# Kernel optimization log

Measured on AMD Instinct MI355X. Metric: run time of the kernel, lower is better.

## Reference

```python
import jax, jax.numpy as jnp
import numpy as np

B, T, D, H = 4, 1024, 1024, 16
DH = D // H
NEG_BIG = jnp.float32(-2.0**32 + 1)


def layer_norm(x, scale, bias, eps=1e-5):
    mean = jnp.mean(x, axis=-1, keepdims=True)
    var = jnp.mean(jnp.square(x - mean), axis=-1, keepdims=True)
    return (x - mean) * jax.lax.rsqrt(var + eps) * scale + bias


def setup_inputs() -> dict:
    key = jax.random.key(0)
    ks = jax.random.split(key, 10)
    s = 0.02
    x = jax.random.normal(ks[0], (B, T, D), jnp.float32)
    mask = jax.random.randint(ks[1], (B, T), 0, 2).astype(jnp.float32)
    return {
        "x": x,
        "mask": mask,
        "wq": jax.random.normal(ks[2], (D, D), jnp.float32) * s,
        "wk": jax.random.normal(ks[3], (D, D), jnp.float32) * s,
        "wv": jax.random.normal(ks[4], (D, D), jnp.float32) * s,
        "w1": jax.random.normal(ks[5], (D, D), jnp.float32) * s,
        "b1": jnp.zeros((D,), jnp.float32),
        "w2": jax.random.normal(ks[6], (D, D), jnp.float32) * s,
        "b2": jnp.zeros((D,), jnp.float32),
        "ln1_s": jnp.ones((D,), jnp.float32),
        "ln1_b": jnp.zeros((D,), jnp.float32),
        "ln2_s": jnp.ones((D,), jnp.float32),
        "ln2_b": jnp.zeros((D,), jnp.float32),
        "ln3_s": jnp.ones((D,), jnp.float32),
        "ln3_b": jnp.zeros((D,), jnp.float32),
    }


def _mask_enc(x, mask, wq, wk, wv, w1, b1, w2, b2,
              ln1_s, ln1_b, ln2_s, ln2_b, ln3_s, ln3_b):
    b, t, d = x.shape
    # --- multi-head attention (hand-rolled, matches torch split/cat trick) ---
    Q = (x @ wq).reshape(b, t, H, DH).transpose(0, 2, 1, 3)  # [B,H,T,dh]
    K = (x @ wk).reshape(b, t, H, DH).transpose(0, 2, 1, 3)
    V = (x @ wv).reshape(b, t, H, DH).transpose(0, 2, 1, 3)
    scores = jnp.einsum('bhqd,bhkd->bhqk', Q, K) / jnp.sqrt(jnp.float32(DH))
    # key padding mask from sign of |K| row sums
    key_m = jnp.sign(jnp.sum(jnp.abs(K), axis=-1))  # [B,H,T]
    scores = jnp.where(key_m[:, :, None, :] == 0, NEG_BIG, scores)
    # FORWARD direction: allowed where col_index > row_index (strict)
    idx = jnp.arange(t)
    allowed = (idx[None, :] > idx[:, None]).astype(scores.dtype)  # [T,T]
    scores = scores + (1.0 - allowed) * (-10000.0)
    attn = jax.nn.softmax(scores, axis=-1)
    # post-softmax query mask multiply
    query_m = jnp.sign(jnp.sum(jnp.abs(Q), axis=-1))[:, :, :, None]  # [B,H,T,1]
    attn = attn * query_m
    out = jnp.einsum('bhqk,bhkd->bhqd', attn, V)
    out = out.transpose(0, 2, 1, 3).reshape(b, t, d)  # combine heads
    out = out * mask[:, :, None]
    # --- residual + layernorm wrapper (attention) ---
    h1 = layer_norm(x + out, ln1_s, ln1_b)
    # --- FFN + residual + layernorm ---
    ffn = jax.nn.relu(h1 @ w1 + b1) @ w2 + b2
    h2 = layer_norm(h1 + ffn, ln2_s, ln2_b)
    # --- output normalization ---
    return layer_norm(h2, ln3_s, ln3_b)


def reference(x, mask, wq, wk, wv, w1, b1, w2, b2,
              ln1_s, ln1_b, ln2_s, ln2_b, ln3_s, ln3_b):
    return _mask_enc(x, mask, wq, wk, wv, w1, b1, w2, b2,
                     ln1_s, ln1_b, ln2_s, ln2_b, ln3_s, ln3_b)
```

## Files before the change

### kernel.cpp

```cpp
#include <hip/hip_runtime.h>
#include <stdint.h>


#define B_  4
#define T_  1024
#define D_  1024
#define H_  16
#define DH_ 64

typedef __attribute__((ext_vector_type(8))) short short8;
typedef __attribute__((ext_vector_type(4))) float floatx4;
typedef __attribute__((ext_vector_type(4))) _Float16 half4;

__device__ __forceinline__ unsigned short f2bf(float f) {
  union { float f; uint32_t u; } a; a.f = f;
  uint32_t r = a.u + 0x7FFFu + ((a.u >> 16) & 1u);
  return (unsigned short)(r >> 16);
}
__device__ __forceinline__ float bf2f(unsigned short u) {
  union { uint32_t u; float f; } a; a.u = ((uint32_t)u) << 16;
  return a.f;
}

#define GLD_LDS16(g, l) __builtin_amdgcn_global_load_lds( \
    (const __attribute__((address_space(1))) unsigned int*)(g), \
    (__attribute__((address_space(3))) unsigned int*)(l), 16, 0, 0)

__global__ __launch_bounds__(256)
void prep_kernel(const float4* __restrict__ x4, unsigned short* __restrict__ xb,
                 const float* __restrict__ w0, const float* __restrict__ w1,
                 const float* __restrict__ w2, const float* __restrict__ w3,
                 const float* __restrict__ w4, unsigned short* __restrict__ dst_all) {
  const int t = threadIdx.x;
  if (blockIdx.x < 4096) {
    int idx = blockIdx.x * 256 + t;
    float4 v = x4[idx];
    union { uint2 u; unsigned short s[4]; } o;
    o.s[0] = f2bf(v.x); o.s[1] = f2bf(v.y); o.s[2] = f2bf(v.z); o.s[3] = f2bf(v.w);
    *(uint2*)&xb[(size_t)idx * 4] = o.u;
    return;
  }
  const int b = blockIdx.x - 4096;
  const int z = b >> 8, ky = (b >> 4) & 15, nx = b & 15;
  const float* src = (z == 0) ? w0 : (z == 1) ? w1 : (z == 2) ? w2 : (z == 3) ? w3 : w4;
  unsigned short* dst = dst_all + (size_t)z * D_ * D_;
  __shared__ __align__(16) unsigned short tile[64 * 72];
  const int k0 = ky * 64, n0 = nx * 64;
#pragma unroll
  for (int c = 0; c < 4; ++c) {
    int idx = c * 256 + t;
    int r = idx >> 4, cc = (idx & 15) << 2;
    float4 v = *(const float4*)&src[(size_t)(k0 + r) * D_ + n0 + cc];
    tile[(cc + 0) * 72 + r] = f2bf(v.x);
    tile[(cc + 1) * 72 + r] = f2bf(v.y);
    tile[(cc + 2) * 72 + r] = f2bf(v.z);
    tile[(cc + 3) * 72 + r] = f2bf(v.w);
  }
  __syncthreads();
  int rr = t >> 2, ck = (t & 3) << 4;
  uint4 v0 = *(const uint4*)&tile[rr * 72 + ck];
  uint4 v1 = *(const uint4*)&tile[rr * 72 + ck + 8];
  *(uint4*)&dst[(size_t)(n0 + rr) * D_ + k0 + ck] = v0;
  *(uint4*)&dst[(size_t)(n0 + rr) * D_ + k0 + ck + 8] = v1;
}

__global__ __launch_bounds__(256, 2)
void gemm_qkv(const unsigned short* __restrict__ A,
              const unsigned short* __restrict__ Bt,
              unsigned short* __restrict__ oQ, unsigned short* __restrict__ oK,
              _Float16* __restrict__ oV) {
  const int K = 1024;
  __shared__ __align__(16) unsigned short As[128 * 32];
  __shared__ __align__(16) unsigned short Bs[128 * 32];
  __shared__ __align__(16) _Float16 Cs[2 * 64 * 136];
  const int t = threadIdx.x;
  const int lane = t & 63, w = t >> 6;
  const int quad = lane >> 4, lm = lane & 15;
  const int wm = w >> 1, wn = w & 1;
  const int m0 = blockIdx.y * 128, n0 = blockIdx.x * 128;
  const int arow = w * 32 + (lane >> 2), acol = (lane & 3) << 3;

  floatx4 acc[4][4];
#pragma unroll
  for (int i = 0; i < 4; ++i)
#pragma unroll
    for (int j = 0; j < 4; ++j) acc[i][j] = (floatx4){0.f, 0.f, 0.f, 0.f};

  for (int kt = 0; kt < K; kt += 32) {
    const unsigned short* ga = A + (size_t)(m0 + arow) * K + kt + acol;
    const unsigned short* gb = Bt + (size_t)(n0 + arow) * K + kt + acol;
    GLD_LDS16(ga, &As[(w * 32) * 32]);
    GLD_LDS16(ga + (size_t)16 * K, &As[(w * 32 + 16) * 32]);
    GLD_LDS16(gb, &Bs[(w * 32) * 32]);
    GLD_LDS16(gb + (size_t)16 * K, &Bs[(w * 32 + 16) * 32]);
    __syncthreads();
    short8 a[4], b[4];
#pragma unroll
    for (int i = 0; i < 4; ++i) a[i] = *(const short8*)&As[(wm * 64 + i * 16 + lm) * 32 + quad * 8];
#pragma unroll
    for (int j = 0; j < 4; ++j) b[j] = *(const short8*)&Bs[(wn * 64 + j * 16 + lm) * 32 + quad * 8];
#pragma unroll
    for (int i = 0; i < 4; ++i)
#pragma unroll
      for (int j = 0; j < 4; ++j)
        acc[i][j] = __builtin_amdgcn_mfma_f32_16x16x32_bf16(a[i], b[j], acc[i][j], 0, 0, 0);
    __syncthreads();
  }

  if (n0 < 2048) {
    unsigned short* p = (n0 < 1024) ? oQ : oK;
    const float qscale = (n0 < 1024) ? 0.18033688f : 1.0f;
#pragma unroll
    for (int i = 0; i < 4; ++i) {
      int gmb = m0 + wm * 64 + i * 16 + quad * 4;
#pragma unroll
      for (int j = 0; j < 4; ++j) {
        int gn = n0 + wn * 64 + j * 16 + lm;
        int nn = gn & 1023, hh = nn >> 6, dd = nn & 63;
#pragma unroll
        for (int r = 0; r < 4; ++r) {
          int gm = gmb + r;
          int bb = gm >> 10, tt = gm & 1023;
          p[(((size_t)bb * H_ + hh) * T_ + tt) * DH_ + dd] = f2bf(acc[i][j][r] * qscale);
        }
      }
    }
  } else {
#pragma unroll
    for (int i = 0; i < 4; ++i) {
#pragma unroll
      for (int j = 0; j < 4; ++j) {
        int gn = n0 + wn * 64 + j * 16 + lm;
        int hd = (gn >> 6) & 1, dd = gn & 63;
        int kperm = quad * 32 + (wm * 4 + i) * 4;
        union { _Float16 h[4]; uint2 u; } pk;
#pragma unroll
        for (int r = 0; r < 4; ++r) pk.h[r] = (_Float16)acc[i][j][r];
        *(uint2*)&Cs[((size_t)(hd * 64 + dd)) * 136 + kperm] = pk.u;
      }
    }
    __syncthreads();
    const int row = t >> 1, half = t & 1;
    const int hd = row >> 6, dd = row & 63;
    const int hh = ((n0 & 1023) >> 6) + hd;
    const int bb = m0 >> 10, kbg = (m0 >> 7) & 7;
    const _Float16* srcp = &Cs[(size_t)(hd * 64 + dd) * 136 + half * 64];
    _Float16* dstp = oV + ((((size_t)bb * H_ + hh) * DH_ + dd) * 8 + kbg) * 128 + half * 64;
#pragma unroll
    for (int g = 0; g < 8; ++g)
      *(uint4*)(dstp + g * 8) = *(const uint4*)(srcp + g * 8);
  }
}

template <int MODE>
__global__ __launch_bounds__(256, 2)
void gemm_ffn(const unsigned short* __restrict__ A,
              const unsigned short* __restrict__ Bt,
              unsigned short* __restrict__ oBf, float* __restrict__ oF,
              const float* __restrict__ bias) {
  const int K = 1024, N = 1024;
  __shared__ __align__(16) unsigned short As[64 * 32];
  __shared__ __align__(16) unsigned short Bs[128 * 32];
  const int t = threadIdx.x;
  const int lane = t & 63, w = t >> 6;
  const int quad = lane >> 4, lm = lane & 15;
  const int wm = w >> 1, wn = w & 1;
  const int m0 = blockIdx.y * 64, n0 = blockIdx.x * 128;
  const int lrow = lane >> 2, lcol = (lane & 3) << 3;

  floatx4 acc[2][4];
#pragma unroll
  for (int i = 0; i < 2; ++i)
#pragma unroll
    for (int j = 0; j < 4; ++j) acc[i][j] = (floatx4){0.f, 0.f, 0.f, 0.f};

  for (int kt = 0; kt < K; kt += 32) {
    const unsigned short* ga = A + (size_t)(m0 + w * 16 + lrow) * K + kt + lcol;
    const unsigned short* gb = Bt + (size_t)(n0 + w * 32 + lrow) * K + kt + lcol;
    GLD_LDS16(ga, &As[(w * 16) * 32]);
    GLD_LDS16(gb, &Bs[(w * 32) * 32]);
    GLD_LDS16(gb + (size_t)16 * K, &Bs[(w * 32 + 16) * 32]);
    __syncthreads();
    short8 a[2], b[4];
#pragma unroll
    for (int i = 0; i < 2; ++i) a[i] = *(const short8*)&As[(wm * 32 + i * 16 + lm) * 32 + quad * 8];
#pragma unroll
    for (int j = 0; j < 4; ++j) b[j] = *(const short8*)&Bs[(wn * 64 + j * 16 + lm) * 32 + quad * 8];
#pragma unroll
    for (int i = 0; i < 2; ++i)
#pragma unroll
      for (int j = 0; j < 4; ++j)
        acc[i][j] = __builtin_amdgcn_mfma_f32_16x16x32_bf16(a[i], b[j], acc[i][j], 0, 0, 0);
    __syncthreads();
  }

#pragma unroll
  for (int i = 0; i < 2; ++i) {
    int gmb = m0 + wm * 32 + i * 16 + quad * 4;
#pragma unroll
    for (int j = 0; j < 4; ++j) {
      int gn = n0 + wn * 64 + j * 16 + lm;
      float bv = bias[gn];
#pragma unroll
      for (int r = 0; r < 4; ++r) {
        int gm = gmb + r;
        float v = acc[i][j][r] + bv;
        if (MODE == 1) {
          oBf[(size_t)gm * N + gn] = f2bf(fmaxf(v, 0.f));
        } else {
          oF[(size_t)gm * N + gn] = v;
        }
      }
    }
  }
}

__global__ __launch_bounds__(256)
void flash_attn(const unsigned short* __restrict__ Qb,
                const unsigned short* __restrict__ Kb,
                const _Float16* __restrict__ Vtg,
                const float* __restrict__ maskp,
                unsigned short* __restrict__ attn) {
  const int t = threadIdx.x;
  const int lane = t & 63, w = t >> 6;
  const int quad = lane >> 4, lm = lane & 15;

  const int bid = blockIdx.x;
  const int xcd = bid & 7;
  const int qslot = (bid >> 3) & 7;
  const int hgrp = bid >> 6;
  const int head = hgrp * 8 + xcd;
  const int qh = qslot >> 1;
  const int qb = (qslot & 1) ? 7 - qh : qh;
  const int hh = head & 15, bb = head >> 4;
  const int q0 = qb << 7;

  const size_t headoff = ((size_t)bb * H_ + hh) * T_ * DH_;
  const unsigned short* Qh = Qb + headoff;
  const unsigned short* Kh = Kb + headoff;
  const _Float16* Vh = Vtg + headoff;

  short8 qf[2][2];
#pragma unroll
  for (int qg = 0; qg < 2; ++qg)
#pragma unroll
    for (int ks = 0; ks < 2; ++ks)
      qf[qg][ks] = *(const short8*)(Qh + (size_t)(q0 + w * 32 + qg * 16 + lm) * 64 + ks * 32 + quad * 8);

  float lsum[2] = {0.f, 0.f};
  floatx4 acc[2][4];
#pragma unroll
  for (int qg = 0; qg < 2; ++qg)
#pragma unroll
    for (int j2 = 0; j2 < 4; ++j2) acc[qg][j2] = (floatx4){0.f, 0.f, 0.f, 0.f};

  const int qglob0 = q0 + w * 32 + lm;
  const bool excl1 = (qglob0 + 16 == 1023);
  const float MSHIFT = 14426.950408f;

  const int kb_lo = (qb == 7 && w == 3) ? 0 : qb;

  short8 kf[8][2];
  {
    const unsigned short* Kblk = Kh + (size_t)(kb_lo * 128) * 64;
#pragma unroll
    for (int j = 0; j < 8; ++j) {
      kf[j][0] = *(const short8*)(Kblk + (size_t)(j * 16 + lm) * 64 + quad * 8);
      kf[j][1] = *(const short8*)(Kblk + (size_t)(j * 16 + lm) * 64 + 32 + quad * 8);
    }
  }

  for (int kb = kb_lo; kb < 8; ++kb) {
    const int k0 = kb * 128;
    const bool need_mask = (kb <= qb);
    const bool has_next = (kb + 1 < 8);
    const unsigned short* Kn = Kh + (size_t)((kb + 1) * 128) * 64;

    union { uint4 u[4]; _Float16 h[32]; } vf[4];
#pragma unroll
    for (int j2 = 0; j2 < 4; ++j2) {
      const _Float16* vp = Vh + ((size_t)(j2 * 16 + lm) * 8 + kb) * 128 + quad * 32;
#pragma unroll
      for (int g = 0; g < 4; ++g) vf[j2].u[g] = *(const uint4*)(vp + g * 8);
    }

#pragma unroll
    for (int j = 0; j < 8; ++j) {
      floatx4 st[2];
#pragma unroll
      for (int qg = 0; qg < 2; ++qg) {
        floatx4 z = (floatx4){0.f, 0.f, 0.f, 0.f};
        z = __builtin_amdgcn_mfma_f32_16x16x32_bf16(kf[j][0], qf[qg][0], z, 0, 0, 0);
        st[qg] = __builtin_amdgcn_mfma_f32_16x16x32_bf16(kf[j][1], qf[qg][1], z, 0, 0, 0);
      }
      if (has_next) {
        kf[j][0] = *(const short8*)(Kn + (size_t)(j * 16 + lm) * 64 + quad * 8);
        kf[j][1] = *(const short8*)(Kn + (size_t)(j * 16 + lm) * 64 + 32 + quad * 8);
      }
      half4 pa[2];
#pragma unroll
      for (int qg = 0; qg < 2; ++qg) {
        const int qq = qglob0 + qg * 16;
        const bool skip = (qg == 1) && excl1;
#pragma unroll
        for (int r = 0; r < 4; ++r) {
          int kg = k0 + j * 16 + quad * 4 + r;
          float v = st[qg][r];
          if (need_mask && !skip && kg <= qq) v -= MSHIFT;
          float p = __builtin_amdgcn_exp2f(v);
          lsum[qg] += p;
          pa[qg][r] = (_Float16)p;
        }
      }
#pragma unroll
      for (int j2 = 0; j2 < 4; ++j2) {
        half4 vb;
#pragma unroll
        for (int r = 0; r < 4; ++r) vb[r] = vf[j2].h[j * 4 + r];
        acc[0][j2] = __builtin_amdgcn_mfma_f32_16x16x16f16(pa[0], vb, acc[0][j2], 0, 0, 0);
        acc[1][j2] = __builtin_amdgcn_mfma_f32_16x16x16f16(pa[1], vb, acc[1][j2], 0, 0, 0);
      }
    }
  }

#pragma unroll
  for (int qg = 0; qg < 2; ++qg) {
    float l = lsum[qg];
    l += __shfl_xor(l, 16);
    l += __shfl_xor(l, 32);
    float s = maskp[bb * T_ + qglob0 + qg * 16] / l;
#pragma unroll
    for (int r = 0; r < 4; ++r) {
      float bsc = __shfl(s, quad * 4 + r);
      int tq = q0 + w * 32 + qg * 16 + quad * 4 + r;
#pragma unroll
      for (int j2 = 0; j2 < 4; ++j2)
        attn[((size_t)(bb * T_ + tq)) * D_ + hh * 64 + j2 * 16 + lm] = f2bf(acc[qg][j2][r] * bsc);
    }
  }
}

__global__ __launch_bounds__(256)
void ln_res_kernel(const float* __restrict__ xa, const unsigned short* __restrict__ attn,
                   const float* __restrict__ sc, const float* __restrict__ bi,
                   float* __restrict__ h, unsigned short* __restrict__ hb) {
  const int row = blockIdx.x, t = threadIdx.x;
  const int lane = t & 63, wid = t >> 6;
  size_t base = (size_t)row * D_ + t * 4;
  float4 a = *(const float4*)&xa[base];
  union { uint2 u; unsigned short s[4]; } au;
  au.u = *(const uint2*)&attn[base];
  float v0 = a.x + bf2f(au.s[0]), v1 = a.y + bf2f(au.s[1]);
  float v2 = a.z + bf2f(au.s[2]), v3 = a.w + bf2f(au.s[3]);
  float s1 = v0 + v1 + v2 + v3;
  float s2 = v0 * v0 + v1 * v1 + v2 * v2 + v3 * v3;
#pragma unroll
  for (int off = 32; off; off >>= 1) { s1 += __shfl_down(s1, off); s2 += __shfl_down(s2, off); }
  __shared__ float r1[4], r2[4];
  if (lane == 0) { r1[wid] = s1; r2[wid] = s2; }
  __syncthreads();
  s1 = r1[0] + r1[1] + r1[2] + r1[3];
  s2 = r2[0] + r2[1] + r2[2] + r2[3];
  float mean = s1 * (1.f / 1024.f);
  float var = s2 * (1.f / 1024.f) - mean * mean;
  float rstd = rsqrtf(var + 1e-5f);
  float4 sv = *(const float4*)&sc[t * 4];
  float4 bv = *(const float4*)&bi[t * 4];
  float o0 = (v0 - mean) * rstd * sv.x + bv.x;
  float o1 = (v1 - mean) * rstd * sv.y + bv.y;
  float o2 = (v2 - mean) * rstd * sv.z + bv.z;
  float o3 = (v3 - mean) * rstd * sv.w + bv.w;
  float4 ov = {o0, o1, o2, o3};
  *(float4*)&h[base] = ov;
  union { uint2 u; unsigned short s[4]; } ob;
  ob.s[0] = f2bf(o0); ob.s[1] = f2bf(o1); ob.s[2] = f2bf(o2); ob.s[3] = f2bf(o3);
  *(uint2*)&hb[base] = ob.u;
}

__global__ __launch_bounds__(256)
void ln_double_kernel(const float* __restrict__ h1, const float* __restrict__ ffn,
                      const float* __restrict__ s2c, const float* __restrict__ b2c,
                      const float* __restrict__ s3c, const float* __restrict__ b3c,
                      float* __restrict__ out) {
  const int row = blockIdx.x, t = threadIdx.x;
  const int lane = t & 63, wid = t >> 6;
  size_t base = (size_t)row * D_ + t * 4;
  float4 a = *(const float4*)&h1[base];
  float4 b = *(const float4*)&ffn[base];
  float v0 = a.x + b.x, v1 = a.y + b.y, v2 = a.z + b.z, v3 = a.w + b.w;
  float s1 = v0 + v1 + v2 + v3;
  float s2 = v0 * v0 + v1 * v1 + v2 * v2 + v3 * v3;
#pragma unroll
  for (int off = 32; off; off >>= 1) { s1 += __shfl_down(s1, off); s2 += __shfl_down(s2, off); }
  __shared__ float ra[4], rb[4], rc[4], rd[4];
  if (lane == 0) { ra[wid] = s1; rb[wid] = s2; }
  __syncthreads();
  s1 = ra[0] + ra[1] + ra[2] + ra[3];
  s2 = rb[0] + rb[1] + rb[2] + rb[3];
  float mean = s1 * (1.f / 1024.f);
  float var = s2 * (1.f / 1024.f) - mean * mean;
  float rstd = rsqrtf(var + 1e-5f);
  float4 sv = *(const float4*)&s2c[t * 4];
  float4 bv = *(const float4*)&b2c[t * 4];
  float o0 = (v0 - mean) * rstd * sv.x + bv.x;
  float o1 = (v1 - mean) * rstd * sv.y + bv.y;
  float o2 = (v2 - mean) * rstd * sv.z + bv.z;
  float o3 = (v3 - mean) * rstd * sv.w + bv.w;
  float u1 = o0 + o1 + o2 + o3;
  float u2 = o0 * o0 + o1 * o1 + o2 * o2 + o3 * o3;
#pragma unroll
  for (int off = 32; off; off >>= 1) { u1 += __shfl_down(u1, off); u2 += __shfl_down(u2, off); }
  if (lane == 0) { rc[wid] = u1; rd[wid] = u2; }
  __syncthreads();
  u1 = rc[0] + rc[1] + rc[2] + rc[3];
  u2 = rd[0] + rd[1] + rd[2] + rd[3];
  float mean2 = u1 * (1.f / 1024.f);
  float var2 = u2 * (1.f / 1024.f) - mean2 * mean2;
  float rstd2 = rsqrtf(var2 + 1e-5f);
  float4 s3v = *(const float4*)&s3c[t * 4];
  float4 b3v = *(const float4*)&b3c[t * 4];
  float4 fo;
  fo.x = (o0 - mean2) * rstd2 * s3v.x + b3v.x;
  fo.y = (o1 - mean2) * rstd2 * s3v.y + b3v.y;
  fo.z = (o2 - mean2) * rstd2 * s3v.z + b3v.z;
  fo.w = (o3 - mean2) * rstd2 * s3v.w + b3v.w;
  *(float4*)&out[base] = fo;
}

extern "C" void kernel_launch(void* const* d_in, const int* in_sizes, int n_in,
                              void* d_out, int out_size, void* d_ws, size_t ws_size,
                              hipStream_t stream) {
  (void)in_sizes; (void)n_in; (void)out_size; (void)ws_size;
  const float* x   = (const float*)d_in[0];
  const float* msk = (const float*)d_in[1];
  const float* wq  = (const float*)d_in[2];
  const float* wk  = (const float*)d_in[3];
  const float* wv  = (const float*)d_in[4];
  const float* w1  = (const float*)d_in[5];
  const float* b1  = (const float*)d_in[6];
  const float* w2  = (const float*)d_in[7];
  const float* b2  = (const float*)d_in[8];
  const float* l1s = (const float*)d_in[9];
  const float* l1b = (const float*)d_in[10];
  const float* l2s = (const float*)d_in[11];
  const float* l2b = (const float*)d_in[12];
  const float* l3s = (const float*)d_in[13];
  const float* l3b = (const float*)d_in[14];
  float* outp = (float*)d_out;

  char* ws = (char*)d_ws;
  unsigned short* xb   = (unsigned short*)(ws);
  unsigned short* wt   = (unsigned short*)(ws + ((size_t)8  << 20));
  unsigned short* Qb   = (unsigned short*)(ws + ((size_t)18 << 20));
  unsigned short* Kb   = (unsigned short*)(ws + ((size_t)26 << 20));
  _Float16*       Vtg  = (_Float16*)(ws + ((size_t)34 << 20));
  unsigned short* attn = (unsigned short*)(ws + ((size_t)42 << 20));
  float* h1            = (float*)(ws + ((size_t)50 << 20));
  unsigned short* h1b  = (unsigned short*)(ws + ((size_t)18 << 20));
  unsigned short* gb   = (unsigned short*)(ws + ((size_t)26 << 20));
  float* ffn           = (float*)(ws + ((size_t)34 << 20));

  prep_kernel<<<4096 + 1280, 256, 0, stream>>>((const float4*)x, xb,
                                               wq, wk, wv, w1, w2, wt);
  gemm_qkv<<<dim3(24, 32), 256, 0, stream>>>(xb, wt, Qb, Kb, Vtg);
  flash_attn<<<512, 256, 0, stream>>>(Qb, Kb, Vtg, msk, attn);
  ln_res_kernel<<<4096, 256, 0, stream>>>(x, attn, l1s, l1b, h1, h1b);
  gemm_ffn<1><<<dim3(8, 64), 256, 0, stream>>>(h1b, wt + (size_t)3 * 1024 * 1024, gb, nullptr, b1);
  gemm_ffn<2><<<dim3(8, 64), 256, 0, stream>>>(gb, wt + (size_t)4 * 1024 * 1024, nullptr, ffn, b2);
  ln_double_kernel<<<4096, 256, 0, stream>>>(h1, ffn, l2s, l2b, l3s, l3b, outp);
}
```

Baseline: 262.2 us.

## Split flash attention into 64-row query tiles to double block count

The attention kernel now gives each block 64 query rows (16 per wave) instead of 128, and launches 1024 blocks instead of 512. The block-to-(head, query tile) mapping is redone so blocks pair short and long causal tiles and stay grouped by XCD. The aim is to fill more of the CUs and balance the triangular workload better. In exchange, each K/V tile is reused by fewer query rows, so K/V loads per unit of compute roughly double.

```diff
diff --git a/kernel.cpp b/kernel.cpp
--- a/kernel.cpp
+++ b/kernel.cpp
@@ -227,38 +227,38 @@
 
   const int bid = blockIdx.x;
   const int xcd = bid & 7;
-  const int qslot = (bid >> 3) & 7;
-  const int hgrp = bid >> 6;
+  const int hgrp = (bid >> 3) & 7;
+  const int qlow = (bid >> 6) & 3;
+  const int qhi  = bid >> 8;
+  const int q1 = qlow * 2 + (qhi & 1);
+  const int qb6 = (qhi >> 1) ? (15 - q1) : q1;
   const int head = hgrp * 8 + xcd;
-  const int qh = qslot >> 1;
-  const int qb = (qslot & 1) ? 7 - qh : qh;
   const int hh = head & 15, bb = head >> 4;
-  const int q0 = qb << 7;
+
+  const int qr0 = qb6 * 64 + w * 16;
+  const int kdiag = qr0 >> 7;
 
   const size_t headoff = ((size_t)bb * H_ + hh) * T_ * DH_;
   const unsigned short* Qh = Qb + headoff;
   const unsigned short* Kh = Kb + headoff;
   const _Float16* Vh = Vtg + headoff;
 
-  short8 qf[2][2];
-#pragma unroll
-  for (int qg = 0; qg < 2; ++qg)
-#pragma unroll
-    for (int ks = 0; ks < 2; ++ks)
-      qf[qg][ks] = *(const short8*)(Qh + (size_t)(q0 + w * 32 + qg * 16 + lm) * 64 + ks * 32 + quad * 8);
-
-  float lsum[2] = {0.f, 0.f};
-  floatx4 acc[2][4];
-#pragma unroll
-  for (int qg = 0; qg < 2; ++qg)
-#pragma unroll
-    for (int j2 = 0; j2 < 4; ++j2) acc[qg][j2] = (floatx4){0.f, 0.f, 0.f, 0.f};
-
-  const int qglob0 = q0 + w * 32 + lm;
-  const bool excl1 = (qglob0 + 16 == 1023);
+  short8 qf[2];
+#pragma unroll
+  for (int ks = 0; ks < 2; ++ks)
+    qf[ks] = *(const short8*)(Qh + (size_t)(qr0 + lm) * 64 + ks * 32 + quad * 8);
+
+  float lsum = 0.f;
+  floatx4 acc[4];
+#pragma unroll
+  for (int j2 = 0; j2 < 4; ++j2) acc[j2] = (floatx4){0.f, 0.f, 0.f, 0.f};
+
+  const int qq = qr0 + lm;
+  const bool excl = (qq == 1023);
   const float MSHIFT = 14426.950408f;
 
-  const int kb_lo = (qb == 7 && w == 3) ? 0 : qb;
+  const bool tail1023 = (qb6 == 15) && (w == 3);
+  const int kb_lo = tail1023 ? 0 : kdiag;
 
   short8 kf[8][2];
   {
@@ -272,7 +272,7 @@
 
   for (int kb = kb_lo; kb < 8; ++kb) {
     const int k0 = kb * 128;
-    const bool need_mask = (kb <= qb);
+    const bool need_mask = (kb <= kdiag);
     const bool has_next = (kb + 1 < 8);
     const unsigned short* Kn = Kh + (size_t)((kb + 1) * 128) * 64;
 
@@ -286,56 +286,48 @@
 
 #pragma unroll
     for (int j = 0; j < 8; ++j) {
-      floatx4 st[2];
-#pragma unroll
-      for (int qg = 0; qg < 2; ++qg) {
+      floatx4 st;
+      {
         floatx4 z = (floatx4){0.f, 0.f, 0.f, 0.f};
-        z = __builtin_amdgcn_mfma_f32_16x16x32_bf16(kf[j][0], qf[qg][0], z, 0, 0, 0);
-        st[qg] = __builtin_amdgcn_mfma_f32_16x16x32_bf16(kf[j][1], qf[qg][1], z, 0, 0, 0);
+        z = __builtin_amdgcn_mfma_f32_16x16x32_bf16(kf[j][0], qf[0], z, 0, 0, 0);
+        st = __builtin_amdgcn_mfma_f32_16x16x32_bf16(kf[j][1], qf[1], st = z, 0, 0, 0);
       }
       if (has_next) {
         kf[j][0] = *(const short8*)(Kn + (size_t)(j * 16 + lm) * 64 + quad * 8);
         kf[j][1] = *(const short8*)(Kn + (size_t)(j * 16 + lm) * 64 + 32 + quad * 8);
       }
-      half4 pa[2];
-#pragma unroll
-      for (int qg = 0; qg < 2; ++qg) {
-        const int qq = qglob0 + qg * 16;
-        const bool skip = (qg == 1) && excl1;
-#pragma unroll
-        for (int r = 0; r < 4; ++r) {
-          int kg = k0 + j * 16 + quad * 4 + r;
-          float v = st[qg][r];
-          if (need_mask && !skip && kg <= qq) v -= MSHIFT;
-          float p = __builtin_amdgcn_exp2f(v);
-          lsum[qg] += p;
-          pa[qg][r] = (_Float16)p;
-        }
+      half4 pa;
+#pragma unroll
+      for (int r = 0; r < 4; ++r) {
+        int kg = k0 + j * 16 + quad * 4 + r;
+        float v = st[r];
+        if (need_mask && !excl && kg <= qq) v -= MSHIFT;
+        float p = __builtin_amdgcn_exp2f(v);
+        lsum += p;
+        pa[r] = (_Float16)p;
       }
 #pragma unroll
       for (int j2 = 0; j2 < 4; ++j2) {
         half4 vb;
 #pragma unroll
         for (int r = 0; r < 4; ++r) vb[r] = vf[j2].h[j * 4 + r];
-        acc[0][j2] = __builtin_amdgcn_mfma_f32_16x16x16f16(pa[0], vb, acc[0][j2], 0, 0, 0);
-        acc[1][j2] = __builtin_amdgcn_mfma_f32_16x16x16f16(pa[1], vb, acc[1][j2], 0, 0, 0);
-      }
-    }
-  }
-
-#pragma unroll
-  for (int qg = 0; qg < 2; ++qg) {
-    float l = lsum[qg];
+        acc[j2] = __builtin_amdgcn_mfma_f32_16x16x16f16(pa, vb, acc[j2], 0, 0, 0);
+      }
+    }
+  }
+
+  {
+    float l = lsum;
     l += __shfl_xor(l, 16);
     l += __shfl_xor(l, 32);
-    float s = maskp[bb * T_ + qglob0 + qg * 16] / l;
+    float s = maskp[bb * T_ + qq] / l;
 #pragma unroll
     for (int r = 0; r < 4; ++r) {
       float bsc = __shfl(s, quad * 4 + r);
-      int tq = q0 + w * 32 + qg * 16 + quad * 4 + r;
+      int tq = qr0 + quad * 4 + r;
 #pragma unroll
       for (int j2 = 0; j2 < 4; ++j2)
-        attn[((size_t)(bb * T_ + tq)) * D_ + hh * 64 + j2 * 16 + lm] = f2bf(acc[qg][j2][r] * bsc);
+        attn[((size_t)(bb * T_ + tq)) * D_ + hh * 64 + j2 * 16 + lm] = f2bf(acc[j2][r] * bsc);
     }
   }
 }
@@ -463,7 +455,7 @@
   prep_kernel<<<4096 + 1280, 256, 0, stream>>>((const float4*)x, xb,
                                                wq, wk, wv, w1, w2, wt);
   gemm_qkv<<<dim3(24, 32), 256, 0, stream>>>(xb, wt, Qb, Kb, Vtg);
-  flash_attn<<<512, 256, 0, stream>>>(Qb, Kb, Vtg, msk, attn);
+  flash_attn<<<1024, 256, 0, stream>>>(Qb, Kb, Vtg, msk, attn);
   ln_res_kernel<<<4096, 256, 0, stream>>>(x, attn, l1s, l1b, h1, h1b);
   gemm_ffn<1><<<dim3(8, 64), 256, 0, stream>>>(h1b, wt + (size_t)3 * 1024 * 1024, gb, nullptr, b1);
   gemm_ffn<2><<<dim3(8, 64), 256, 0, stream>>>(gb, wt + (size_t)4 * 1024 * 1024, nullptr, ffn, b2);
```

New measurement: 282.6 us. 1.08x slower.
